# Kernel optimization log

Hardware: AMD Instinct MI355X
Metric: run time of the kernel (lower is better)

Reference implementation:

```python
import jax, jax.numpy as jnp
import numpy as np

B, N, DIM, H, DH = 2, 2048, 1024, 16, 64
ALPHA = 32.0 ** 2  # stable_softmax alpha
SCALE = DH ** -0.5


def rotate_half(x):
    # interleaved pairs: (x0, x1, x2, x3, ...) -> (-x1, x0, -x3, x2, ...)
    xp = x.reshape(x.shape[:-1] + (-1, 2))
    return jnp.stack((-xp[..., 1], xp[..., 0]), axis=-1).reshape(x.shape)


def apply_rotary(freqs, t):
    # freqs: [n, d]; t: [b, h, n, d]
    return t * jnp.cos(freqs) + rotate_half(t) * jnp.sin(freqs)


def setup_inputs() -> dict:
    key = jax.random.key(0)
    k0, k1, k2, k3 = jax.random.split(key, 4)
    x = jax.random.normal(k0, (B, N, DIM), jnp.float32)
    rotary_pos_emb = jax.random.normal(k1, (N, DH), jnp.float32)
    w_qkv = jax.random.normal(k2, (DIM, 3 * H * DH), jnp.float32) / np.sqrt(DIM)
    w_out = jax.random.normal(k3, (H * DH, DIM), jnp.float32) / np.sqrt(H * DH)
    b_out = jnp.zeros((DIM,), jnp.float32)
    return {"x": x, "rotary_pos_emb": rotary_pos_emb, "w_qkv": w_qkv,
            "w_out": w_out, "b_out": b_out}


def reference(x, rotary_pos_emb, w_qkv, w_out, b_out):
    b, n, _ = x.shape
    qkv = x @ w_qkv                                  # [b, n, 3*h*d]
    q, k, v = jnp.split(qkv, 3, axis=-1)
    to_heads = lambda t: t.reshape(b, n, H, DH).transpose(0, 2, 1, 3)  # [b,h,n,d]
    q, k, v = map(to_heads, (q, k, v))
    freqs = rotary_pos_emb[:n]
    # source applies rotary emb to q, k AND v
    q = apply_rotary(freqs, q)
    k = apply_rotary(freqs, k)
    v = apply_rotary(freqs, v)
    q = q * SCALE
    dots = jnp.einsum('bhid,bhjd->bhij', q, k)       # [b,h,n,n]
    mask_value = -jnp.finfo(dots.dtype).max
    causal = jnp.triu(jnp.ones((n, n), bool), 1)
    dots = jnp.where(causal, mask_value, dots)
    # stable softmax: divide by alpha, subtract detached max, rescale
    t = dots / ALPHA
    t = t - jax.lax.stop_gradient(jnp.max(t, axis=-1, keepdims=True))
    attn = jax.nn.softmax(t * ALPHA, axis=-1)
    out = jnp.einsum('bhij,bhjd->bhid', attn, v)     # [b,h,n,d]
    out = out.transpose(0, 2, 1, 3).reshape(b, n, H * DH)
    return out @ w_out + b_out
```

## Files before the change

### kernel.cpp

```cpp
#include <hip/hip_runtime.h>
#include <stdint.h>

#define DEV __device__ __forceinline__

typedef __bf16 bf16x8 __attribute__((ext_vector_type(8)));
typedef float  f32x4  __attribute__((ext_vector_type(4)));
typedef short  s16x8  __attribute__((ext_vector_type(8)));

constexpr int Bb   = 2;
constexpr int Nn   = 2048;
constexpr int DIMc = 1024;
constexpr int Hh   = 16;
constexpr int DHc  = 64;
constexpr int BN   = Bb * Nn;
constexpr int QKVC = 3 * Hh * DHc;

DEV ushort f2b(float f) {
  uint32_t u = __float_as_uint(f);
  u += 0x7fffu + ((u >> 16) & 1u);
  return (ushort)(u >> 16);
}

DEV void gload16(const void* g, void* l) {
  __builtin_amdgcn_global_load_lds(
      (const __attribute__((address_space(1))) void*)(uintptr_t)g,
      (__attribute__((address_space(3))) void*)(uint32_t)(uintptr_t)l,
      16, 0, 0);
}

DEV f32x4 mfma16(bf16x8 a, bf16x8 b, f32x4 c) {
  return __builtin_amdgcn_mfma_f32_16x16x32_bf16(a, b, c, 0, 0, 0);
}

DEV uint32_t cvtpk(float lo, float hi) {
  uint32_t r;
  asm("v_cvt_pk_bf16_f32 %0, %1, %2" : "=v"(r) : "v"(lo), "v"(hi));
  return r;
}


__global__ void k_cast_x(const float* __restrict__ x, ushort* __restrict__ xb) {
  int i = blockIdx.x * 256 + threadIdx.x;
  size_t base = (size_t)i * 8;
  s16x8 v;
#pragma unroll
  for (int j = 0; j < 8; ++j) v[j] = (short)f2b(x[base + j]);
  *(s16x8*)(xb + base) = v;
}

__global__ void k_sincos(const float* __restrict__ rope,
                         float* __restrict__ cosT, float* __restrict__ sinT) {
  int i = blockIdx.x * 256 + threadIdx.x;
  float t = rope[i];
  float s, c;
  sincosf(t, &s, &c);
  cosT[i] = c;
  sinT[i] = s;
}

__global__ void k_transpose_cast(const float* __restrict__ src, ushort* __restrict__ dst,
                                 int K, int Ncols) {
  __shared__ float tile[32][33];
  int nb = blockIdx.x * 32, kb = blockIdx.y * 32;
  int tx = threadIdx.x, ty = threadIdx.y;
#pragma unroll
  for (int i = 0; i < 4; ++i) {
    int k = ty + i * 8;
    tile[k][tx] = src[(size_t)(kb + k) * Ncols + nb + tx];
  }
  __syncthreads();
#pragma unroll
  for (int i = 0; i < 4; ++i) {
    int n = ty + i * 8;
    dst[(size_t)(nb + n) * K + kb + tx] = f2b(tile[tx][n]);
  }
}

DEV void gemm_core(const ushort* __restrict__ A, const ushort* __restrict__ Bt,
                   int rowBase, int colBase, ushort* lA, ushort* lB,
                   f32x4 (&acc)[4][4]) {
  const int tid = threadIdx.x;
  const int lane = tid & 63, w = tid >> 6;
  const int wm = w >> 1, wn = w & 1;
  const int g = lane >> 4, l16 = lane & 15;
  const f32x4 zero = {0.f, 0.f, 0.f, 0.f};
#pragma unroll
  for (int i = 0; i < 4; ++i)
#pragma unroll
    for (int j = 0; j < 4; ++j) acc[i][j] = zero;

  for (int k0 = 0; k0 < DIMc; k0 += 32) {
#pragma unroll
    for (int s = 0; s < 2; ++s) {
      int c = s * 256 + tid;
      int row = c >> 2, kc = c & 3;
      gload16(A  + (size_t)(rowBase + row) * DIMc + k0 + kc * 8,
              lA + (size_t)(s * 256 + w * 64) * 8);
      gload16(Bt + (size_t)(colBase + row) * DIMc + k0 + kc * 8,
              lB + (size_t)(s * 256 + w * 64) * 8);
    }
    __syncthreads();
    bf16x8 af[4], bfr[4];
#pragma unroll
    for (int f = 0; f < 4; ++f)
      af[f] = *(const bf16x8*)&lA[(wm * 64 + f * 16 + l16) * 32 + g * 8];
#pragma unroll
    for (int f = 0; f < 4; ++f)
      bfr[f] = *(const bf16x8*)&lB[(wn * 64 + f * 16 + l16) * 32 + g * 8];
#pragma unroll
    for (int i = 0; i < 4; ++i)
#pragma unroll
      for (int j = 0; j < 4; ++j)
        acc[i][j] = mfma16(af[i], bfr[j], acc[i][j]);
    __syncthreads();
  }
}

__global__ __launch_bounds__(256) void k_gemm_qkv(
    const ushort* __restrict__ xb, const ushort* __restrict__ wT,
    const float* __restrict__ cosT, const float* __restrict__ sinT,
    ushort* __restrict__ Qd, ushort* __restrict__ Kd, ushort* __restrict__ Vd) {
  __shared__ ushort lA[128 * 32];
  __shared__ ushort lB[128 * 32];
  f32x4 acc[4][4];
  const int rowBase = blockIdx.y * 128, colBase = blockIdx.x * 128;
  gemm_core(xb, wT, rowBase, colBase, lA, lB, acc);

  const int lane = threadIdx.x & 63, w = threadIdx.x >> 6;
  const int wm = w >> 1, wn = w & 1;
  const int g = lane >> 4, l16 = lane & 15;
#pragma unroll
  for (int fm = 0; fm < 4; ++fm) {
#pragma unroll
    for (int fn = 0; fn < 4; ++fn) {
      int col = colBase + wn * 64 + fn * 16 + l16;
      int sel = col >> 10, hc = col & 1023;
      int h = hc >> 6, d = hc & 63;
      float sgn = (d & 1) ? 1.f : -1.f;
#pragma unroll
      for (int r = 0; r < 4; ++r) {
        float t  = acc[fm][fn][r];
        float tp = __shfl_xor(t, 1);
        int row = rowBase + wm * 64 + fm * 16 + 4 * g + r;
        int b = row >> 11, n = row & 2047;
        float cv = cosT[n * 64 + d], sv = sinT[n * 64 + d];
        float rv = t * cv + sgn * tp * sv;
        if (sel == 0) {
          Qd[((size_t)(b * Hh + h) * Nn + n) * DHc + d] = f2b(rv * 0.125f);
        } else if (sel == 1) {
          Kd[((size_t)(b * Hh + h) * Nn + n) * DHc + d] = f2b(rv);
        } else {
          Vd[((size_t)(b * Hh + h) * DHc + d) * Nn + n] = f2b(rv);
        }
      }
    }
  }
}


DEV void stageKV(const ushort* __restrict__ Kh, const ushort* __restrict__ Vh,
                 ushort* lKb, ushort* lVb, int kt, int tid, int w) {
#pragma unroll
  for (int s = 0; s < 2; ++s) {
    int c = s * 256 + tid;
    int row = c >> 3, jst = c & 7;
    int jl = jst ^ (row & 7);
    gload16(Kh + (size_t)(kt * 64 + row) * DHc + jl * 8,
            lKb + (size_t)(s * 256 + w * 64) * 8);
    gload16(Vh + (size_t)row * Nn + kt * 64 + jl * 8,
            lVb + (size_t)(s * 256 + w * 64) * 8);
  }
}

DEV void attn_step(const ushort* lKc, const ushort* lVc, char* lPw,
                   const bf16x8 (&q)[2], f32x4 (&o)[4], float& m, float& l,
                   int kBase, int qg, bool diag, int g, int l16) {
  const f32x4 zero = {0.f, 0.f, 0.f, 0.f};
  f32x4 s[4];
#pragma unroll
  for (int jt = 0; jt < 4; ++jt) s[jt] = zero;

#pragma unroll
  for (int jt = 0; jt < 4; ++jt) {
    int jr = jt * 16 + l16;
#pragma unroll
    for (int d0 = 0; d0 < 2; ++d0) {
      bf16x8 kb = *(const bf16x8*)&lKc[jr * 64 + (((d0 * 4 + g) ^ (jr & 7)) << 3)];
      s[jt] = mfma16(kb, q[d0], s[jt]);
    }
  }

  if (diag) {
#pragma unroll
    for (int jt = 0; jt < 4; ++jt)
#pragma unroll
      for (int r = 0; r < 4; ++r) {
        int j = kBase + jt * 16 + 4 * g + r;
        if (j > qg) s[jt][r] = -3.0e38f;
      }
  }

  float tmax = fmaxf(fmaxf(fmaxf(s[0][0], s[0][1]), fmaxf(s[0][2], s[0][3])),
                     fmaxf(fmaxf(s[1][0], s[1][1]), fmaxf(s[1][2], s[1][3])));
  tmax = fmaxf(tmax, fmaxf(fmaxf(fmaxf(s[2][0], s[2][1]), fmaxf(s[2][2], s[2][3])),
                           fmaxf(fmaxf(s[3][0], s[3][1]), fmaxf(s[3][2], s[3][3]))));
  tmax = fmaxf(tmax, __shfl_xor(tmax, 16));
  tmax = fmaxf(tmax, __shfl_xor(tmax, 32));

  if (!__all(tmax <= m + 8.f)) {
    float mnew = fmaxf(m, tmax);
    float sc = __expf(m - mnew);
#pragma unroll
    for (int dt = 0; dt < 4; ++dt) o[dt] *= sc;
    l *= sc;
    m = mnew;
  }

  float ps = 0.f;
#pragma unroll
  for (int jt = 0; jt < 4; ++jt)
#pragma unroll
    for (int r = 0; r < 4; ++r) {
      float p = __expf(s[jt][r] - m);
      s[jt][r] = p;
      ps += p;
    }
  ps += __shfl_xor(ps, 16);
  ps += __shfl_xor(ps, 32);
  l += ps;

  const int sw = (l16 & 7) << 4;
  char* prow = lPw + l16 * 128;
#pragma unroll
  for (int jt = 0; jt < 4; ++jt) {
    int jo = (jt * 16 + 4 * g) * 2;
    *(uint32_t*)(prow + (jo ^ sw))       = cvtpk(s[jt][0], s[jt][1]);
    *(uint32_t*)(prow + ((jo + 4) ^ sw)) = cvtpk(s[jt][2], s[jt][3]);
  }

  bf16x8 pa[2];
#pragma unroll
  for (int jh = 0; jh < 2; ++jh)
    pa[jh] = *(const bf16x8*)(prow + (((jh * 32 + 8 * g) * 2) ^ sw));
#pragma unroll
  for (int dt = 0; dt < 4; ++dt) {
    int d = dt * 16 + l16;
#pragma unroll
    for (int jh = 0; jh < 2; ++jh) {
      bf16x8 vb = *(const bf16x8*)&lVc[d * 64 + (((jh * 4 + g) ^ (d & 7)) << 3)];
      o[dt] = mfma16(vb, pa[jh], o[dt]);
    }
  }
}

DEV void attn_epi(ushort* __restrict__ ao, int bh, int n, int g,
                  f32x4 (&o)[4], float l) {
  const int b = bh >> 4, h = bh & 15;
  float inv = 1.f / l;
  ushort* dst = ao + (size_t)(b * Nn + n) * (Hh * DHc) + h * 64;
#pragma unroll
  for (int dt = 0; dt < 4; ++dt) {
    uint2 pkd;
    pkd.x = cvtpk(o[dt][0] * inv, o[dt][1] * inv);
    pkd.y = cvtpk(o[dt][2] * inv, o[dt][3] * inv);
    *(uint2*)(dst + dt * 16 + 4 * g) = pkd;
  }
}

__global__ __launch_bounds__(256) void k_attn(
    const ushort* __restrict__ Qd, const ushort* __restrict__ Kd,
    const ushort* __restrict__ Vd, ushort* __restrict__ ao) {
  __shared__ ushort lK[2][64 * 64];
  __shared__ ushort lV[2][64 * 64];
  __shared__ char   lP[4][16 * 128];
  const int tid = threadIdx.x;
  const int lane = tid & 63, w = tid >> 6;
  const int g = lane >> 4, l16 = lane & 15;
  const int bh = blockIdx.y;
  const int p = blockIdx.x;
  const int tA = p, tB = 31 - p;
  const int last = tB;
  const ushort* Qh = Qd + (size_t)bh * Nn * DHc;
  const ushort* Kh = Kd + (size_t)bh * Nn * DHc;
  const ushort* Vh = Vd + (size_t)bh * DHc * Nn;

  const int qgA = tA * 64 + w * 16 + l16;
  const int qgB = tB * 64 + w * 16 + l16;

  bf16x8 qA[2], qB[2];
#pragma unroll
  for (int d0 = 0; d0 < 2; ++d0) {
    qA[d0] = *(const bf16x8*)(Qh + (size_t)qgA * DHc + d0 * 32 + g * 8);
    qB[d0] = *(const bf16x8*)(Qh + (size_t)qgB * DHc + d0 * 32 + g * 8);
  }

  const f32x4 zero = {0.f, 0.f, 0.f, 0.f};
  f32x4 oA[4], oB[4];
#pragma unroll
  for (int dt = 0; dt < 4; ++dt) { oA[dt] = zero; oB[dt] = zero; }
  float mA = -3.0e38f, lA_ = 0.f, mB = -3.0e38f, lB_ = 0.f;

  stageKV(Kh, Vh, lK[0], lV[0], 0, tid, w);

  for (int kt = 0; kt <= last; ++kt) {
    const int cur = kt & 1;
    if (kt < last) {
      stageKV(Kh, Vh, lK[cur ^ 1], lV[cur ^ 1], kt + 1, tid, w);
      asm volatile("s_waitcnt vmcnt(4)" ::: "memory");
    } else {
      asm volatile("s_waitcnt vmcnt(0)" ::: "memory");
    }
    __builtin_amdgcn_s_barrier();

    attn_step(lK[cur], lV[cur], lP[w], qB, oB, mB, lB_, kt * 64, qgB, kt == tB, g, l16);
    if (kt <= tA)
      attn_step(lK[cur], lV[cur], lP[w], qA, oA, mA, lA_, kt * 64, qgA, kt == tA, g, l16);

    __builtin_amdgcn_s_barrier();
  }

  attn_epi(ao, bh, qgA, g, oA, lA_);
  attn_epi(ao, bh, qgB, g, oB, lB_);
}

__global__ __launch_bounds__(256) void k_gemm_out(
    const ushort* __restrict__ ao, const ushort* __restrict__ wT,
    const float* __restrict__ bias, float* __restrict__ out) {
  __shared__ ushort lA[128 * 32];
  __shared__ ushort lB[128 * 32];
  f32x4 acc[4][4];
  const int rowBase = blockIdx.y * 128, colBase = blockIdx.x * 128;
  gemm_core(ao, wT, rowBase, colBase, lA, lB, acc);

  const int lane = threadIdx.x & 63, w = threadIdx.x >> 6;
  const int wm = w >> 1, wn = w & 1;
  const int g = lane >> 4, l16 = lane & 15;
#pragma unroll
  for (int fm = 0; fm < 4; ++fm)
#pragma unroll
    for (int fn = 0; fn < 4; ++fn) {
      int col = colBase + wn * 64 + fn * 16 + l16;
#pragma unroll
      for (int r = 0; r < 4; ++r) {
        int row = rowBase + wm * 64 + fm * 16 + 4 * g + r;
        out[(size_t)row * DIMc + col] = acc[fm][fn][r] + bias[col];
      }
    }
}

extern "C" void kernel_launch(void* const* d_in, const int* in_sizes, int n_in,
                              void* d_out, int out_size, void* d_ws, size_t ws_size,
                              hipStream_t stream) {
  const float* x     = (const float*)d_in[0];
  const float* rope  = (const float*)d_in[1];
  const float* w_qkv = (const float*)d_in[2];
  const float* w_out = (const float*)d_in[3];
  const float* b_out = (const float*)d_in[4];
  float* out = (float*)d_out;

  char* ws = (char*)d_ws;
  ushort* xb    = (ushort*)(ws);
  ushort* wqkvT = (ushort*)(ws + 8388608);
  ushort* woutT = (ushort*)(ws + 14680064);
  float*  cosT  = (float*) (ws + 16777216);
  float*  sinT  = (float*) (ws + 17301504);
  ushort* Qd    = (ushort*)(ws + 17825792);
  ushort* Kd    = (ushort*)(ws + 26214400);
  ushort* Vd    = (ushort*)(ws + 34603008);
  ushort* ao    = (ushort*)(ws + 42991616);

  hipLaunchKernelGGL(k_cast_x, dim3(2048), dim3(256), 0, stream, x, xb);
  hipLaunchKernelGGL(k_transpose_cast, dim3(QKVC / 32, DIMc / 32), dim3(32, 8), 0, stream,
                     w_qkv, wqkvT, DIMc, QKVC);
  hipLaunchKernelGGL(k_transpose_cast, dim3(DIMc / 32, DIMc / 32), dim3(32, 8), 0, stream,
                     w_out, woutT, DIMc, DIMc);
  hipLaunchKernelGGL(k_sincos, dim3(Nn * DHc / 256), dim3(256), 0, stream, rope, cosT, sinT);
  hipLaunchKernelGGL(k_gemm_qkv, dim3(QKVC / 128, BN / 128), dim3(256), 0, stream,
                     xb, wqkvT, cosT, sinT, Qd, Kd, Vd);
  hipLaunchKernelGGL(k_attn, dim3(16, Bb * Hh), dim3(256), 0, stream, Qd, Kd, Vd, ao);
  hipLaunchKernelGGL(k_gemm_out, dim3(DIMc / 128, BN / 128), dim3(256), 0, stream,
                     ao, woutT, b_out, out);
}
```

Before: 138.0 us.

## Double-buffer GEMM LDS tiles with prefetch and XOR swizzle; pack cos/sin

The shared GEMM core now keeps two LDS buffers and issues global-to-LDS loads for the next K slice before computing the current one, waiting with vmcnt instead of a full sync. This overlaps load latency with MFMA work. LDS chunk positions are XOR-swizzled by row to cut bank conflicts on the fragment reads. The rope cos and sin tables are interleaved into one float2 array so the QKV epilogue does a single load. LDS use per block doubles, which may lower occupancy.

Result: no change. 135.6 us (-1.8%).

```diff
diff --git a/kernel.cpp b/kernel.cpp
--- a/kernel.cpp
+++ b/kernel.cpp
@@ -48,14 +48,12 @@
   *(s16x8*)(xb + base) = v;
 }
 
-__global__ void k_sincos(const float* __restrict__ rope,
-                         float* __restrict__ cosT, float* __restrict__ sinT) {
+__global__ void k_sincos(const float* __restrict__ rope, float2* __restrict__ csT) {
   int i = blockIdx.x * 256 + threadIdx.x;
   float t = rope[i];
   float s, c;
   sincosf(t, &s, &c);
-  cosT[i] = c;
-  sinT[i] = s;
+  csT[i] = make_float2(c, s);
 }
 
 __global__ void k_transpose_cast(const float* __restrict__ src, ushort* __restrict__ dst,
@@ -89,39 +87,63 @@
 #pragma unroll
     for (int j = 0; j < 4; ++j) acc[i][j] = zero;
 
+  const int c0row = tid >> 2,          c0kc = (tid & 3) ^ ((c0row >> 1) & 3);
+  const int c1row = (256 + tid) >> 2,  c1kc = (tid & 3) ^ ((c1row >> 1) & 3);
+  const ushort* gA0 = A  + (size_t)(rowBase + c0row) * DIMc + c0kc * 8;
+  const ushort* gA1 = A  + (size_t)(rowBase + c1row) * DIMc + c1kc * 8;
+  const ushort* gB0 = Bt + (size_t)(colBase + c0row) * DIMc + c0kc * 8;
+  const ushort* gB1 = Bt + (size_t)(colBase + c1row) * DIMc + c1kc * 8;
+  ushort* lDst0 = (ushort*)((size_t)(0 * 256 + w * 64) * 8 * 2);
+  const size_t o0 = (size_t)(0 * 256 + w * 64) * 8;
+  const size_t o1 = (size_t)(1 * 256 + w * 64) * 8;
+
+  gload16(gA0, lA + o0);
+  gload16(gB0, lB + o0);
+  gload16(gA1, lA + o1);
+  gload16(gB1, lB + o1);
+
   for (int k0 = 0; k0 < DIMc; k0 += 32) {
-#pragma unroll
-    for (int s = 0; s < 2; ++s) {
-      int c = s * 256 + tid;
-      int row = c >> 2, kc = c & 3;
-      gload16(A  + (size_t)(rowBase + row) * DIMc + k0 + kc * 8,
-              lA + (size_t)(s * 256 + w * 64) * 8);
-      gload16(Bt + (size_t)(colBase + row) * DIMc + k0 + kc * 8,
-              lB + (size_t)(s * 256 + w * 64) * 8);
-    }
-    __syncthreads();
+    const int cur = (k0 >> 5) & 1;
+    ushort* cA = lA + cur * (128 * 32);
+    ushort* cB = lB + cur * (128 * 32);
+    if (k0 + 32 < DIMc) {
+      ushort* nA = lA + (cur ^ 1) * (128 * 32);
+      ushort* nB = lB + (cur ^ 1) * (128 * 32);
+      int kn = k0 + 32;
+      gload16(gA0 + kn, nA + o0);
+      gload16(gB0 + kn, nB + o0);
+      gload16(gA1 + kn, nA + o1);
+      gload16(gB1 + kn, nB + o1);
+      asm volatile("s_waitcnt vmcnt(4)" ::: "memory");
+    } else {
+      asm volatile("s_waitcnt vmcnt(0)" ::: "memory");
+    }
+    __builtin_amdgcn_s_barrier();
+
     bf16x8 af[4], bfr[4];
 #pragma unroll
-    for (int f = 0; f < 4; ++f)
-      af[f] = *(const bf16x8*)&lA[(wm * 64 + f * 16 + l16) * 32 + g * 8];
-#pragma unroll
-    for (int f = 0; f < 4; ++f)
-      bfr[f] = *(const bf16x8*)&lB[(wn * 64 + f * 16 + l16) * 32 + g * 8];
+    for (int f = 0; f < 4; ++f) {
+      int r  = wm * 64 + f * 16 + l16;
+      int r2 = wn * 64 + f * 16 + l16;
+      af[f]  = *(const bf16x8*)&cA[r * 32 + ((g ^ ((r >> 1) & 3)) << 3)];
+      bfr[f] = *(const bf16x8*)&cB[r2 * 32 + ((g ^ ((r2 >> 1) & 3)) << 3)];
+    }
 #pragma unroll
     for (int i = 0; i < 4; ++i)
 #pragma unroll
       for (int j = 0; j < 4; ++j)
         acc[i][j] = mfma16(af[i], bfr[j], acc[i][j]);
-    __syncthreads();
+
+    __builtin_amdgcn_s_barrier();
   }
 }
 
 __global__ __launch_bounds__(256) void k_gemm_qkv(
     const ushort* __restrict__ xb, const ushort* __restrict__ wT,
-    const float* __restrict__ cosT, const float* __restrict__ sinT,
+    const float2* __restrict__ csT,
     ushort* __restrict__ Qd, ushort* __restrict__ Kd, ushort* __restrict__ Vd) {
-  __shared__ ushort lA[128 * 32];
-  __shared__ ushort lB[128 * 32];
+  __shared__ ushort lA[2 * 128 * 32];
+  __shared__ ushort lB[2 * 128 * 32];
   f32x4 acc[4][4];
   const int rowBase = blockIdx.y * 128, colBase = blockIdx.x * 128;
   gemm_core(xb, wT, rowBase, colBase, lA, lB, acc);
@@ -143,8 +165,8 @@
         float tp = __shfl_xor(t, 1);
         int row = rowBase + wm * 64 + fm * 16 + 4 * g + r;
         int b = row >> 11, n = row & 2047;
-        float cv = cosT[n * 64 + d], sv = sinT[n * 64 + d];
-        float rv = t * cv + sgn * tp * sv;
+        float2 cs = csT[n * 64 + d];
+        float rv = t * cs.x + sgn * tp * cs.y;
         if (sel == 0) {
           Qd[((size_t)(b * Hh + h) * Nn + n) * DHc + d] = f2b(rv * 0.125f);
         } else if (sel == 1) {
@@ -326,8 +348,8 @@
 __global__ __launch_bounds__(256) void k_gemm_out(
     const ushort* __restrict__ ao, const ushort* __restrict__ wT,
     const float* __restrict__ bias, float* __restrict__ out) {
-  __shared__ ushort lA[128 * 32];
-  __shared__ ushort lB[128 * 32];
+  __shared__ ushort lA[2 * 128 * 32];
+  __shared__ ushort lB[2 * 128 * 32];
   f32x4 acc[4][4];
   const int rowBase = blockIdx.y * 128, colBase = blockIdx.x * 128;
   gemm_core(ao, wT, rowBase, colBase, lA, lB, acc);
@@ -362,8 +384,7 @@
   ushort* xb    = (ushort*)(ws);
   ushort* wqkvT = (ushort*)(ws + 8388608);
   ushort* woutT = (ushort*)(ws + 14680064);
-  float*  cosT  = (float*) (ws + 16777216);
-  float*  sinT  = (float*) (ws + 17301504);
+  float2* csT   = (float2*)(ws + 16777216);
   ushort* Qd    = (ushort*)(ws + 17825792);
   ushort* Kd    = (ushort*)(ws + 26214400);
   ushort* Vd    = (ushort*)(ws + 34603008);
@@ -374,9 +395,9 @@
                      w_qkv, wqkvT, DIMc, QKVC);
   hipLaunchKernelGGL(k_transpose_cast, dim3(DIMc / 32, DIMc / 32), dim3(32, 8), 0, stream,
                      w_out, woutT, DIMc, DIMc);
-  hipLaunchKernelGGL(k_sincos, dim3(Nn * DHc / 256), dim3(256), 0, stream, rope, cosT, sinT);
+  hipLaunchKernelGGL(k_sincos, dim3(Nn * DHc / 256), dim3(256), 0, stream, rope, csT);
   hipLaunchKernelGGL(k_gemm_qkv, dim3(QKVC / 128, BN / 128), dim3(256), 0, stream,
-                     xb, wqkvT, cosT, sinT, Qd, Kd, Vd);
+                     xb, wqkvT, csT, Qd, Kd, Vd);
   hipLaunchKernelGGL(k_attn, dim3(16, Bb * Hh), dim3(256), 0, stream, Qd, Kd, Vd, ao);
   hipLaunchKernelGGL(k_gemm_out, dim3(DIMc / 128, BN / 128), dim3(256), 0, stream,
                      ao, woutT, b_out, out);
```
